# Performance work log

Hardware: AMD Instinct MI355X
Metric: run time of the kernel (lower is better)

Reference implementation:

```python
import jax, jax.numpy as jnp
import numpy as np

B, T, D, H = 8, 1024, 512, 8
DK = D // H


def setup_inputs() -> dict:
    key = jax.random.key(0)
    ks = jax.random.split(key, 6)
    s = 0.02
    return {
        "inputs": jax.random.normal(ks[0], (B, T, D), jnp.float32),
        "ln1_g": jnp.ones((D,), jnp.float32),
        "ln1_b": jnp.zeros((D,), jnp.float32),
        "ln2_g": jnp.ones((D,), jnp.float32),
        "ln2_b": jnp.zeros((D,), jnp.float32),
        "W_qkv": jax.random.normal(ks[1], (3 * D, D), jnp.float32) * s,
        "W_pos": jax.random.normal(ks[2], (D, D), jnp.float32) * s,
        "W_out": jax.random.normal(ks[3], (D, D), jnp.float32) * s,
        "b_out": jnp.zeros((D,), jnp.float32),
        "pos_bias_u": jax.random.normal(ks[4], (H, DK), jnp.float32) * s,
        "pos_bias_v": jax.random.normal(ks[5], (H, DK), jnp.float32) * s,
    }


def layer_norm(x, g, b, eps=1e-5):
    mu = jnp.mean(x, axis=-1, keepdims=True)
    var = jnp.var(x, axis=-1, keepdims=True)
    return (x - mu) * jax.lax.rsqrt(var + eps) * g + b


def rel_shift(x):
    # x: (b, h, t1, t2); Transformer-XL pad-reshape-slice relative shift
    b, h, t1, t2 = x.shape
    xp = jnp.pad(x, ((0, 0), (0, 0), (0, 0), (1, 0)))  # zero col at front
    xp = xp.reshape(b, h, t2 + 1, t1)[:, :, 1:, :]
    return xp.reshape(b, h, t1, t2)


def reference(inputs, ln1_g, ln1_b, ln2_g, ln2_b, W_qkv, W_pos, W_out, b_out,
              pos_bias_u, pos_bias_v):
    b, t, d = inputs.shape
    # PositionalEmbedding: pos_seq is the literal data values inputs[0,:,0]
    pos_seq = inputs[0, :, 0]
    inv_freq = 1.0 / (10000.0 ** (jnp.arange(0, d, 2, dtype=jnp.float32) / d))
    sin_inp = pos_seq[:, None] * inv_freq[None, :]  # (T, D/2)
    pos_emb = jnp.concatenate([jnp.sin(sin_inp), jnp.cos(sin_inp)], axis=-1)  # (T, D)
    # outer layer norm, then inner layer norm inside forward_qkv
    x = layer_norm(inputs, ln1_g, ln1_b)
    xn = layer_norm(x, ln2_g, ln2_b)
    qkv = xn @ W_qkv.T  # (B, T, 3D)
    q, k, v = jnp.split(qkv, 3, axis=-1)
    q = q.reshape(b, t, H, DK)                       # (B, T, H, DK)
    k = k.reshape(b, t, H, DK).transpose(0, 2, 1, 3)  # (B, H, T, DK)
    v = v.reshape(b, t, H, DK).transpose(0, 2, 1, 3)  # (B, H, T, DK)
    p = (pos_emb @ W_pos.T).reshape(t, H, DK)         # (T, H, DK), pos batch = 1
    qu = (q + pos_bias_u).transpose(0, 2, 1, 3)       # (B, H, T, DK)
    qv = (q + pos_bias_v).transpose(0, 2, 1, 3)
    ac = jnp.einsum('bhqd,bhkd->bhqk', qu, k)
    bd = jnp.einsum('bhqd,khd->bhqk', qv, p)
    bd = rel_shift(bd)
    scores = (ac + bd) / jnp.sqrt(jnp.float32(DK))
    attn = jax.nn.softmax(scores, axis=-1)
    out = jnp.einsum('bhqk,bhkd->bqhd', attn, v).reshape(b, t, d)
    return out @ W_out.T + b_out
```

## Files before the change

kernel.cpp:

```cpp
#include <hip/hip_runtime.h>
#include <stdint.h>

#define B_ 8
#define T_ 1024
#define D_ 512
#define H_ 8
#define DK_ 64
#define M_ (B_*T_)

#define PREP_CAST_BLKS (5 * D_ * D_ / 4 / 256)
#define PREP_POS_BLKS  (T_)
#define PREP_LN_BLKS   (M_)
#define PREP_BLKS      (PREP_CAST_BLKS + PREP_POS_BLKS + PREP_LN_BLKS)

typedef unsigned short u16;
typedef __attribute__((ext_vector_type(8))) short bf16x8;
typedef __attribute__((ext_vector_type(4))) float f32x4;

static __device__ __forceinline__ u16 f2bf(float f) {
  union { float f; unsigned u; } v; v.f = f;
  unsigned r = (v.u + 0x7fffu + ((v.u >> 16) & 1u)) >> 16;
  return (u16)r;
}
static __device__ __forceinline__ u16 f2bf_ru(float f) {
  union { float f; unsigned u; } v; v.f = f;
  return (u16)((v.u + 0x8000u) >> 16);
}
static __device__ __forceinline__ float bf2f(u16 u) {
  union { unsigned u; float f; } v; v.u = ((unsigned)u) << 16;
  return v.f;
}
static __device__ __forceinline__ void async16(const u16* g, u16* l) {
  __builtin_amdgcn_global_load_lds(
      (const __attribute__((address_space(1))) void*)g,
      (__attribute__((address_space(3))) void*)l, 16, 0, 0);
}
static __device__ __forceinline__ f32x4 mfma16(bf16x8 a, bf16x8 b, f32x4 c) {
  return __builtin_amdgcn_mfma_f32_16x16x32_bf16(a, b, c, 0, 0, 0);
}

__global__ __launch_bounds__(256)
void prep_k(const float* __restrict__ wq, const float* __restrict__ wp,
            const float* __restrict__ wo, u16* __restrict__ dq,
            u16* __restrict__ dp, u16* __restrict__ dwo,
            const float* __restrict__ x, u16* __restrict__ pe,
            const float* __restrict__ g1, const float* __restrict__ b1,
            const float* __restrict__ g2, const float* __restrict__ b2,
            u16* __restrict__ xn) {
  __shared__ float red[16];
  const int blk = blockIdx.x;
  const int t = threadIdx.x;
  if (blk < PREP_CAST_BLKS) {
    const int na = 3 * D_ * D_ / 4, nb = D_ * D_ / 4;
    int i = blk * 256 + t;
    const float* s; u16* d; int j;
    if (i < na) { s = wq; d = dq; j = i; }
    else if (i < na + nb) { s = wp; d = dp; j = i - na; }
    else { s = wo; d = dwo; j = i - na - nb; }
    float4 v = ((const float4*)s)[j];
    ushort4 o;
    o.x = f2bf(v.x); o.y = f2bf(v.y); o.z = f2bf(v.z); o.w = f2bf(v.w);
    ((ushort4*)d)[j] = o;
  } else if (blk < PREP_CAST_BLKS + PREP_POS_BLKS) {
    const int tt = blk - PREP_CAST_BLKS;
    float pos = x[(size_t)tt * D_];
    float invf = expf(-(2.f * t / (float)D_) * 9.210340371976184f);
    float ang = pos * invf;
    pe[(size_t)tt * D_ + t] = f2bf(sinf(ang));
    pe[(size_t)tt * D_ + 256 + t] = f2bf(cosf(ang));
  } else {
    const int row = blk - PREP_CAST_BLKS - PREP_POS_BLKS;
    const float2 v = *(const float2*)(x + (size_t)row * D_ + t * 2);
    float a = v.x + v.y;
    float b = v.x * v.x + v.y * v.y;
    for (int off = 32; off; off >>= 1) { a += __shfl_down(a, off, 64); b += __shfl_down(b, off, 64); }
    if ((t & 63) == 0) { red[t >> 6] = a; red[8 + (t >> 6)] = b; }
    __syncthreads();
    a = red[0] + red[1] + red[2] + red[3];
    b = red[8] + red[9] + red[10] + red[11];
    float mu = a * (1.f / D_);
    float var = b * (1.f / D_) - mu * mu;
    float rs = rsqrtf(var + 1e-5f);
    const float2 g1v = *(const float2*)(g1 + t * 2);
    const float2 b1v = *(const float2*)(b1 + t * 2);
    float y0 = (v.x - mu) * rs * g1v.x + b1v.x;
    float y1 = (v.y - mu) * rs * g1v.y + b1v.y;
    __syncthreads();
    a = y0 + y1;
    b = y0 * y0 + y1 * y1;
    for (int off = 32; off; off >>= 1) { a += __shfl_down(a, off, 64); b += __shfl_down(b, off, 64); }
    if ((t & 63) == 0) { red[t >> 6] = a; red[8 + (t >> 6)] = b; }
    __syncthreads();
    a = red[0] + red[1] + red[2] + red[3];
    b = red[8] + red[9] + red[10] + red[11];
    mu = a * (1.f / D_);
    var = b * (1.f / D_) - mu * mu;
    rs = rsqrtf(var + 1e-5f);
    const float2 g2v = *(const float2*)(g2 + t * 2);
    const float2 b2v = *(const float2*)(b2 + t * 2);
    u16* o = xn + (size_t)row * D_ + t * 2;
    o[0] = f2bf((y0 - mu) * rs * g2v.x + b2v.x);
    o[1] = f2bf((y1 - mu) * rs * g2v.y + b2v.y);
  }
}

template<int MODE>
__global__ __launch_bounds__(256, 2)
void gemm_k(const u16* __restrict__ A, const u16* __restrict__ Bw,
            int M, int N, int K,
            u16* __restrict__ o0, u16* __restrict__ o1, u16* __restrict__ o2,
            float* __restrict__ fo, const float* __restrict__ bo) {
  __shared__ u16 As[2][128 * 32];
  __shared__ u16 Bs[2][128 * 32];
  const int tid = threadIdx.x;
  const int l = tid & 63, w = tid >> 6;
  const int m0 = blockIdx.x * 128, n0 = blockIdx.y * 128;
  const int wm = (w >> 1) * 64, wn = (w & 1) * 64;
  const int nk = K >> 5;

  auto stage = [&](int bufi, int kt) {
    const int row = tid >> 2;
    const int cg = ((tid & 3) ^ ((row + (row >> 2)) & 3)) * 8;
    const u16* ga = A + (size_t)(m0 + row) * K + kt * 32 + cg;
    u16* la = &As[bufi][tid * 8];
    async16(ga, la);
    async16(ga + (size_t)64 * K, la + 64 * 32);
    const u16* gb = Bw + (size_t)(n0 + row) * K + kt * 32 + cg;
    u16* lb = &Bs[bufi][tid * 8];
    async16(gb, lb);
    async16(gb + (size_t)64 * K, lb + 64 * 32);
  };

  const int fl = (((l & 15) + ((l & 15) >> 2)) & 3);
  const int coff = ((l >> 4) ^ fl) * 8;
  const int aoff = (l & 15) * 32 + coff;

  f32x4 acc[4][4] = {};
  stage(0, 0);
  for (int kt = 0; kt < nk; ++kt) {
    __syncthreads();
    if (kt + 1 < nk) stage((kt + 1) & 1, kt + 1);
    const u16* as = As[kt & 1];
    const u16* bs = Bs[kt & 1];
    bf16x8 af[4], bfr[4];
#pragma unroll
    for (int i = 0; i < 4; ++i)
      af[i] = *(const bf16x8*)&as[(wm + i * 16) * 32 + aoff];
#pragma unroll
    for (int j = 0; j < 4; ++j)
      bfr[j] = *(const bf16x8*)&bs[(wn + j * 16) * 32 + aoff];
#pragma unroll
    for (int i = 0; i < 4; ++i)
#pragma unroll
      for (int j = 0; j < 4; ++j)
        acc[i][j] = mfma16(af[i], bfr[j], acc[i][j]);
  }

#pragma unroll
  for (int i = 0; i < 4; ++i)
#pragma unroll
    for (int j = 0; j < 4; ++j) {
      const int row0 = m0 + wm + i * 16 + ((l >> 4) << 2);
      const int col = n0 + wn + j * 16 + (l & 15);
      if (MODE == 0) {
        const int sec = col >> 9, cc = col & 511;
        const int hh = cc >> 6, dk = cc & 63;
        const int bb = row0 >> 10, t0r = row0 & 1023;
        if (sec == 2) {
          ushort4 v4;
          v4.x = f2bf(acc[i][j][0]); v4.y = f2bf(acc[i][j][1]);
          v4.z = f2bf(acc[i][j][2]); v4.w = f2bf(acc[i][j][3]);
          *(ushort4*)&o2[((size_t)(bb * H_ + hh) * DK_ + dk) * T_ + t0r] = v4;
        } else {
          u16* dst = (sec == 0) ? o0 : o1;
#pragma unroll
          for (int r = 0; r < 4; ++r)
            dst[((size_t)(bb * H_ + hh) * T_ + t0r + r) * DK_ + dk] = f2bf(acc[i][j][r]);
        }
      } else if (MODE == 1) {
        const int hh = col >> 6, dk = col & 63;
#pragma unroll
        for (int r = 0; r < 4; ++r)
          o0[((size_t)hh * T_ + row0 + r) * DK_ + dk] = f2bf(acc[i][j][r]);
      } else {
#pragma unroll
        for (int r = 0; r < 4; ++r)
          fo[(size_t)(row0 + r) * D_ + col] = acc[i][j][r] + bo[col];
      }
    }
}

__global__ __launch_bounds__(512)
void attn_k(const u16* __restrict__ q, const u16* __restrict__ kb,
            const u16* __restrict__ vt, const u16* __restrict__ pb,
            const float* __restrict__ bu, const float* __restrict__ bv,
            u16* __restrict__ ao) {
  __shared__ u16 k_lds[64 * 64];
  __shared__ u16 v_lds[64 * 64];
  __shared__ u16 pm_lds[192 * 64];
  __shared__ u16 px_lds[128 * 64];
  __shared__ u16 pscr[8][16 * 72];

  const int tid = threadIdx.x;
  const int l = tid & 63, w = tid >> 6;
  const int dd = blockIdx.x;
  const int bh = (dd & 7) * 8 + ((dd >> 3) & 7);
  const int qg = dd >> 6;
  const int q0 = qg * 128;
  const int qbA = qg * 2, qbB = qg * 2 + 1;
  const int b = bh >> 3, h = bh & 7;
  const int diagKt = qbA + (w >> 2);

  const u16* qB = q + (size_t)bh * T_ * DK_;
  const u16* kB = kb + (size_t)bh * T_ * DK_;
  const u16* vB = vt + (size_t)bh * DK_ * T_;
  const u16* pB2 = pb + (size_t)h * T_ * DK_ - 65 * DK_;

  const float SCALE = 0.125f * 1.4426950408889634f;

  bf16x8 quf[2], qvf[2], qsf[2];
  {
    const float* buH = bu + h * DK_;
    const float* bvH = bv + h * DK_;
    const int row = q0 + w * 16 + (l & 15);
    const int row2 = (row + 1 < T_) ? row + 1 : T_ - 1;
    const int ko = (l >> 4) * 8;
    const bf16x8 qa0 = *(const bf16x8*)(qB + (size_t)row * DK_ + ko);
    const bf16x8 qa1 = *(const bf16x8*)(qB + (size_t)row * DK_ + ko + 32);
    const bf16x8 qs0 = *(const bf16x8*)(qB + (size_t)row2 * DK_ + ko);
    const bf16x8 qs1 = *(const bf16x8*)(qB + (size_t)row2 * DK_ + ko + 32);
#pragma unroll
    for (int jj = 0; jj < 8; ++jj) {
      float f0 = bf2f((u16)qa0[jj]), f1 = bf2f((u16)qa1[jj]);
      float g0 = bf2f((u16)qs0[jj]), g1 = bf2f((u16)qs1[jj]);
      float u0 = buH[ko + jj], u1 = buH[ko + 32 + jj];
      float v0 = bvH[ko + jj], v1 = bvH[ko + 32 + jj];
      quf[0][jj] = (short)f2bf((f0 + u0) * SCALE);
      quf[1][jj] = (short)f2bf((f1 + u1) * SCALE);
      qvf[0][jj] = (short)f2bf((f0 + v0) * SCALE);
      qvf[1][jj] = (short)f2bf((f1 + v1) * SCALE);
      qsf[0][jj] = (short)f2bf((g0 + v0) * SCALE);
      qsf[1][jj] = (short)f2bf((g1 + v1) * SCALE);
    }
  }

  f32x4 o[4] = {};
  float lrun[4] = {0.f, 0.f, 0.f, 0.f};
  float sv[4][4];

  const int rbase = 112 - w * 16;
  const int rbaseX = 48 - (w & 3) * 16;
  u16* pwv = &pscr[w][0];
  const int lrow = l & 15;
  const int c0s = ((l >> 4) ^ (l & 7)) * 8;
  const int c1s = c0s ^ 32;
  const int qrow0 = (l >> 4) * 4;

  int srcb[4], hi[4];
#pragma unroll
  for (int r = 0; r < 4; ++r) {
    int d = lrow - qrow0 - r + 15;
    srcb[r] = (((l >> 4) * 16 + (d & 15)) << 2);
    hi[r] = d >> 4;
  }

  const int rr = tid >> 3;
  const int cb = (tid & 7) * 8;
  const int swz = ((tid & 7) ^ (rr & 7)) * 8;
  const int wdst = rr * 64 + swz;
  const unsigned kOffE = (unsigned)(rr * DK_ + cb);
  const unsigned vOffE = (unsigned)(rr * T_ + cb);

  uint4 kreg, vreg, pm0, pm1, pm2, px0, px1;
  auto loadK = [&](int t) { kreg = *(const uint4*)(kB + kOffE + (unsigned)(t * 64 * DK_)); };
  auto loadV = [&](int t) { vreg = *(const uint4*)(vB + vOffE + (unsigned)(t * 64)); };
  auto loadPM = [&](int jb) {
    const unsigned base = kOffE + (unsigned)((jb + 65) * DK_);
    pm0 = *(const uint4*)(pB2 + base);
    pm1 = *(const uint4*)(pB2 + base + 64u * DK_);
    pm2 = *(const uint4*)(pB2 + base + 128u * DK_);
  };
  auto loadPX = [&](int jb) {
    const unsigned base = kOffE + (unsigned)((jb + 65) * DK_);
    px0 = *(const uint4*)(pB2 + base);
    px1 = *(const uint4*)(pB2 + base + 64u * DK_);
  };
  auto mainJb = [&](int t) {
    return (t <= qbA) ? (T_ - 128 + t * 64 - q0) : (t * 64 - q0 - 129);
  };

  loadK(0); loadV(0); loadPM(mainJb(0));
  if (qbA == 0) loadPX(-65);

  for (int kt = 0; kt < 16; ++kt) {
    const bool transA = (kt == qbA), transB = (kt == qbB);
    const bool mainLower = (kt <= qbA);
    const bool mainMask = mainLower ? (kt == diagKt) : (kt <= diagKt + 1);
    const bool myExtra = (transA && w < 4) || (transB && w >= 4);
    const int k0 = kt * 64;

    __syncthreads();
    *(uint4*)&k_lds[wdst] = kreg;
    *(uint4*)&v_lds[wdst] = vreg;
    *(uint4*)&pm_lds[wdst] = pm0;
    *(uint4*)&pm_lds[wdst + 64 * 64] = pm1;
    *(uint4*)&pm_lds[wdst + 128 * 64] = pm2;
    if (transA || transB) {
      *(uint4*)&px_lds[wdst] = px0;
      *(uint4*)&px_lds[wdst + 64 * 64] = px1;
    }
    asm volatile("s_waitcnt lgkmcnt(0)" ::: "memory");
    __builtin_amdgcn_sched_barrier(0);
    __builtin_amdgcn_s_barrier();
    __builtin_amdgcn_sched_barrier(0);

    if (kt < 15) {
      const int t = kt + 1;
      loadK(t); loadV(t); loadPM(mainJb(t));
      if (t == qbA) loadPX(-65);
      else if (t == qbB) loadPX(T_ - 64);
    }

    {
      __builtin_amdgcn_s_setprio(1);
#pragma unroll
      for (int nf = 0; nf < 4; ++nf) {
        const u16* kb0 = &k_lds[(nf * 16 + lrow) * 64];
        bf16x8 b0 = *(const bf16x8*)(kb0 + c0s);
        bf16x8 b1 = *(const bf16x8*)(kb0 + c1s);
        f32x4 acs = {};
        acs = mfma16(quf[0], b0, acs);
        acs = mfma16(quf[1], b1, acs);
#pragma unroll
        for (int r = 0; r < 4; ++r) sv[nf][r] = acs[r];
      }
      __builtin_amdgcn_s_setprio(0);
    }

    {
      bf16x8 A0, A1;
      if (mainLower) { A0 = qvf[0]; A1 = qvf[1]; } else { A0 = qsf[0]; A1 = qsf[1]; }
      f32x4 c[5];
      __builtin_amdgcn_s_setprio(1);
#pragma unroll
      for (int fu = 0; fu < 5; ++fu) {
        const u16* pb0 = &pm_lds[(rbase + fu * 16 + lrow) * 64];
        bf16x8 p0 = *(const bf16x8*)(pb0 + c0s);
        bf16x8 p1 = *(const bf16x8*)(pb0 + c1s);
        f32x4 cc = {};
        cc = mfma16(A0, p0, cc);
        cc = mfma16(A1, p1, cc);
        c[fu] = cc;
      }
      __builtin_amdgcn_s_setprio(0);
#pragma unroll
      for (int r = 0; r < 4; ++r) {
        float rot[5];
#pragma unroll
        for (int fu = 0; fu < 5; ++fu)
          rot[fu] = __int_as_float(
              __builtin_amdgcn_ds_bpermute(srcb[r], __float_as_int(c[fu][r])));
#pragma unroll
        for (int nf = 0; nf < 4; ++nf) {
          float bd = hi[r] ? rot[nf + 1] : rot[nf];
          if (mainMask) {
            int rel = (k0 + nf * 16 + lrow) - (q0 + w * 16 + qrow0 + r);
            bool ok = mainLower ? (rel <= 0) : (rel >= 2);
            bd = ok ? bd : 0.f;
          }
          sv[nf][r] += bd;
        }
      }
    }

    if (myExtra) {
      bf16x8 A0, A1;
      if (w < 4) { A0 = qsf[0]; A1 = qsf[1]; } else { A0 = qvf[0]; A1 = qvf[1]; }
      f32x4 c[5];
      __builtin_amdgcn_s_setprio(1);
#pragma unroll
      for (int fu = 0; fu < 5; ++fu) {
        const u16* pb0 = &px_lds[(rbaseX + fu * 16 + lrow) * 64];
        bf16x8 p0 = *(const bf16x8*)(pb0 + c0s);
        bf16x8 p1 = *(const bf16x8*)(pb0 + c1s);
        f32x4 cc = {};
        cc = mfma16(A0, p0, cc);
        cc = mfma16(A1, p1, cc);
        c[fu] = cc;
      }
      __builtin_amdgcn_s_setprio(0);
#pragma unroll
      for (int r = 0; r < 4; ++r) {
        float rot[5];
#pragma unroll
        for (int fu = 0; fu < 5; ++fu)
          rot[fu] = __int_as_float(
              __builtin_amdgcn_ds_bpermute(srcb[r], __float_as_int(c[fu][r])));
#pragma unroll
        for (int nf = 0; nf < 4; ++nf) {
          float bd = hi[r] ? rot[nf + 1] : rot[nf];
          int rel = (k0 + nf * 16 + lrow) - (q0 + w * 16 + qrow0 + r);
          bool ok = (w < 4) ? (rel >= 2) : (rel <= 0);
          sv[nf][r] += ok ? bd : 0.f;
        }
      }
    }

    {
#pragma unroll
      for (int nf = 0; nf < 4; ++nf)
#pragma unroll
        for (int r = 0; r < 4; ++r)
          sv[nf][r] = __builtin_amdgcn_exp2f(sv[nf][r]);
#pragma unroll
      for (int r = 0; r < 4; ++r)
        lrun[r] += (sv[0][r] + sv[1][r]) + (sv[2][r] + sv[3][r]);

#pragma unroll
      for (int nf = 0; nf < 4; ++nf)
#pragma unroll
        for (int r = 0; r < 4; ++r)
          pwv[(qrow0 + r) * 72 + nf * 16 + lrow] = f2bf_ru(sv[nf][r]);

      bf16x8 pa0 = *(const bf16x8*)&pwv[lrow * 72 + (l >> 4) * 8];
      bf16x8 pa1 = *(const bf16x8*)&pwv[lrow * 72 + 32 + (l >> 4) * 8];
      __builtin_amdgcn_s_setprio(1);
#pragma unroll
      for (int df = 0; df < 4; ++df) {
        const u16* vb2 = &v_lds[(df * 16 + lrow) * 64];
        bf16x8 v0 = *(const bf16x8*)(vb2 + c0s);
        bf16x8 v1 = *(const bf16x8*)(vb2 + c1s);
        o[df] = mfma16(pa0, v0, o[df]);
        o[df] = mfma16(pa1, v1, o[df]);
      }
      __builtin_amdgcn_s_setprio(0);
    }
  }

#pragma unroll
  for (int r = 0; r < 4; ++r) {
#pragma unroll
    for (int off = 1; off < 16; off <<= 1) lrun[r] += __shfl_xor(lrun[r], off, 64);
    lrun[r] = 1.f / lrun[r];
  }
#pragma unroll
  for (int df = 0; df < 4; ++df)
#pragma unroll
    for (int r = 0; r < 4; ++r) {
      int qq = q0 + w * 16 + (l >> 4) * 4 + r;
      int dk = df * 16 + (l & 15);
      float val = o[df][r] * lrun[r];
      ao[((size_t)b * T_ + qq) * D_ + h * DK_ + dk] = f2bf(val);
    }
}

extern "C" void kernel_launch(void* const* d_in, const int* in_sizes, int n_in,
                              void* d_out, int out_size, void* d_ws, size_t ws_size,
                              hipStream_t stream) {
  const float* inputs = (const float*)d_in[0];
  const float* ln1_g = (const float*)d_in[1];
  const float* ln1_b = (const float*)d_in[2];
  const float* ln2_g = (const float*)d_in[3];
  const float* ln2_b = (const float*)d_in[4];
  const float* W_qkv = (const float*)d_in[5];
  const float* W_pos = (const float*)d_in[6];
  const float* W_out = (const float*)d_in[7];
  const float* b_out = (const float*)d_in[8];
  const float* pbu = (const float*)d_in[9];
  const float* pbv = (const float*)d_in[10];
  float* out = (float*)d_out;

  char* ws = (char*)d_ws;
  size_t off = 0;
  auto alloc = [&](size_t bytes) {
    char* p = ws + off;
    off += (bytes + 255) & ~(size_t)255;
    return p;
  };
  u16* xn   = (u16*)alloc((size_t)M_ * D_ * 2);
  u16* wqkv = (u16*)alloc((size_t)3 * D_ * D_ * 2);
  u16* wpos = (u16*)alloc((size_t)D_ * D_ * 2);
  u16* wout = (u16*)alloc((size_t)D_ * D_ * 2);
  u16* pemb = (u16*)alloc((size_t)T_ * D_ * 2);
  u16* qB   = (u16*)alloc((size_t)M_ * D_ * 2);
  u16* kbB  = (u16*)alloc((size_t)M_ * D_ * 2);
  u16* vtB  = (u16*)alloc((size_t)M_ * D_ * 2);
  u16* pbuf = (u16*)alloc((size_t)H_ * T_ * DK_ * 2);
  u16* aoB  = (u16*)alloc((size_t)M_ * D_ * 2);
  if (ws_size < off) return;

  prep_k<<<PREP_BLKS, 256, 0, stream>>>(W_qkv, W_pos, W_out, wqkv, wpos, wout,
                                        inputs, pemb, ln1_g, ln1_b, ln2_g, ln2_b, xn);
  gemm_k<1><<<dim3(T_ / 128, D_ / 128), 256, 0, stream>>>(
      pemb, wpos, T_, D_, D_, pbuf, nullptr, nullptr, nullptr, nullptr);
  gemm_k<0><<<dim3(M_ / 128, (3 * D_) / 128), 256, 0, stream>>>(
      xn, wqkv, M_, 3 * D_, D_, qB, kbB, vtB, nullptr, nullptr);
  attn_k<<<512, 512, 0, stream>>>(qB, kbB, vtB, pbuf, pbu, pbv, aoB);
  gemm_k<2><<<dim3(M_ / 128, D_ / 128), 256, 0, stream>>>(
      aoB, wout, M_, D_, D_, nullptr, nullptr, nullptr, out, b_out);
}
```

Baseline: 140.1 us.

## Load positional band fragments directly from global into registers, dropping LDS staging

The attention kernel no longer stages the relative-position projection rows through shared memory. Each wave loads just its own 5x16-row band of P straight from global memory into bf16x8 registers, prefetching the next tile's band after the current MFMAs. The extra transition-tile band is now read from global inline. This cuts LDS footprint and LDS write/read traffic, which may raise occupancy, but adds redundant global/L2 reads, register pressure, and exposed latency on the extra path.

Measured after the change: 155.0 us. 10.6% more time.

```diff
diff --git a/kernel.cpp b/kernel.cpp
--- a/kernel.cpp
+++ b/kernel.cpp
@@ -197,8 +197,6 @@
             u16* __restrict__ ao) {
   __shared__ u16 k_lds[64 * 64];
   __shared__ u16 v_lds[64 * 64];
-  __shared__ u16 pm_lds[192 * 64];
-  __shared__ u16 px_lds[128 * 64];
   __shared__ u16 pscr[8][16 * 72];
 
   const int tid = threadIdx.x;
@@ -271,26 +269,25 @@
   const unsigned kOffE = (unsigned)(rr * DK_ + cb);
   const unsigned vOffE = (unsigned)(rr * T_ + cb);
 
-  uint4 kreg, vreg, pm0, pm1, pm2, px0, px1;
+  uint4 kreg, vreg;
   auto loadK = [&](int t) { kreg = *(const uint4*)(kB + kOffE + (unsigned)(t * 64 * DK_)); };
   auto loadV = [&](int t) { vreg = *(const uint4*)(vB + vOffE + (unsigned)(t * 64)); };
-  auto loadPM = [&](int jb) {
-    const unsigned base = kOffE + (unsigned)((jb + 65) * DK_);
-    pm0 = *(const uint4*)(pB2 + base);
-    pm1 = *(const uint4*)(pB2 + base + 64u * DK_);
-    pm2 = *(const uint4*)(pB2 + base + 128u * DK_);
-  };
-  auto loadPX = [&](int jb) {
-    const unsigned base = kOffE + (unsigned)((jb + 65) * DK_);
-    px0 = *(const uint4*)(pB2 + base);
-    px1 = *(const uint4*)(pB2 + base + 64u * DK_);
-  };
   auto mainJb = [&](int t) {
     return (t <= qbA) ? (T_ - 128 + t * 64 - q0) : (t * 64 - q0 - 129);
   };
 
-  loadK(0); loadV(0); loadPM(mainJb(0));
-  if (qbA == 0) loadPX(-65);
+  const u16* pwBase = pB2 + (size_t)(65 + rbase + lrow) * DK_ + (l >> 4) * 8;
+  bf16x8 bp0[5], bp1[5];
+  auto loadBand = [&](int jb) {
+#pragma unroll
+    for (int fu = 0; fu < 5; ++fu) {
+      const u16* p = pwBase + (jb + fu * 16) * DK_;
+      bp0[fu] = *(const bf16x8*)p;
+      bp1[fu] = *(const bf16x8*)(p + 32);
+    }
+  };
+
+  loadK(0); loadV(0); loadBand(mainJb(0));
 
   for (int kt = 0; kt < 16; ++kt) {
     const bool transA = (kt == qbA), transB = (kt == qbB);
@@ -302,24 +299,12 @@
     __syncthreads();
     *(uint4*)&k_lds[wdst] = kreg;
     *(uint4*)&v_lds[wdst] = vreg;
-    *(uint4*)&pm_lds[wdst] = pm0;
-    *(uint4*)&pm_lds[wdst + 64 * 64] = pm1;
-    *(uint4*)&pm_lds[wdst + 128 * 64] = pm2;
-    if (transA || transB) {
-      *(uint4*)&px_lds[wdst] = px0;
-      *(uint4*)&px_lds[wdst + 64 * 64] = px1;
-    }
     asm volatile("s_waitcnt lgkmcnt(0)" ::: "memory");
     __builtin_amdgcn_sched_barrier(0);
     __builtin_amdgcn_s_barrier();
     __builtin_amdgcn_sched_barrier(0);
 
-    if (kt < 15) {
-      const int t = kt + 1;
-      loadK(t); loadV(t); loadPM(mainJb(t));
-      if (t == qbA) loadPX(-65);
-      else if (t == qbB) loadPX(T_ - 64);
-    }
+    if (kt < 15) { loadK(kt + 1); loadV(kt + 1); }
 
     {
       __builtin_amdgcn_s_setprio(1);
@@ -344,15 +329,13 @@
       __builtin_amdgcn_s_setprio(1);
 #pragma unroll
       for (int fu = 0; fu < 5; ++fu) {
-        const u16* pb0 = &pm_lds[(rbase + fu * 16 + lrow) * 64];
-        bf16x8 p0 = *(const bf16x8*)(pb0 + c0s);
-        bf16x8 p1 = *(const bf16x8*)(pb0 + c1s);
         f32x4 cc = {};
-        cc = mfma16(A0, p0, cc);
-        cc = mfma16(A1, p1, cc);
+        cc = mfma16(A0, bp0[fu], cc);
+        cc = mfma16(A1, bp1[fu], cc);
         c[fu] = cc;
       }
       __builtin_amdgcn_s_setprio(0);
+      if (kt < 15) loadBand(mainJb(kt + 1));
 #pragma unroll
       for (int r = 0; r < 4; ++r) {
         float rot[5];
@@ -376,13 +359,15 @@
     if (myExtra) {
       bf16x8 A0, A1;
       if (w < 4) { A0 = qsf[0]; A1 = qsf[1]; } else { A0 = qvf[0]; A1 = qvf[1]; }
+      const int jbx = (w < 4) ? -65 : (T_ - 64);
+      const u16* pxBase = pB2 + (size_t)(65 + jbx + rbaseX + lrow) * DK_ + (l >> 4) * 8;
       f32x4 c[5];
       __builtin_amdgcn_s_setprio(1);
 #pragma unroll
       for (int fu = 0; fu < 5; ++fu) {
-        const u16* pb0 = &px_lds[(rbaseX + fu * 16 + lrow) * 64];
-        bf16x8 p0 = *(const bf16x8*)(pb0 + c0s);
-        bf16x8 p1 = *(const bf16x8*)(pb0 + c1s);
+        const u16* p = pxBase + fu * 16 * DK_;
+        bf16x8 p0 = *(const bf16x8*)p;
+        bf16x8 p1 = *(const bf16x8*)(p + 32);
         f32x4 cc = {};
         cc = mfma16(A0, p0, cc);
         cc = mfma16(A1, p1, cc);
```
